# Optimization experiments

Measured on AMD Instinct MI355X. Metric: run time of the kernel, lower is better.

Reference implementation:

```python
import jax, jax.numpy as jnp
import numpy as np

B, S = 4096, 8192

def setup_inputs() -> dict:
    key = jax.random.key(0)
    c = jax.random.normal(key, (B, S), dtype=jnp.float32)
    beta = jnp.asarray(10.0, dtype=jnp.float32)
    return {"c": c, "beta": beta}

def reference(c, beta):
    # Original per-step recurrence:
    #   delta_i = (1/beta) * logsumexp([beta*delta_{i-1}, beta*(c_i + delta_{i-1})])
    #           = delta_{i-1} + (1/beta) * log(1 + exp(beta * c_i))
    # i.e. an exact prefix sum of softplus(beta*c)/beta along S.
    # (Note: the torch code stacks delta_prev, not 0, as the first branch,
    #  so the logsumexp telescopes to a cumulative sum.)
    step = jax.nn.softplus(beta * c) / beta          # (B, S)
    return jnp.cumsum(step, axis=1)                  # (B, S) propagated delays
```

## Files before the change

### kernel.cpp

```cpp
#include <hip/hip_runtime.h>


#define ROW_S   8192
#define NJ      4
#define PASS_F4 (64 * NJ)
#define NPASS   (ROW_S / (PASS_F4 * 4))
#define WPB     4
#define BLOCK_T (WPB * 64)

typedef float f32x4 __attribute__((ext_vector_type(4)));

__device__ __forceinline__ float softplus_step(float c, float beta, float inv_beta) {
    float tb = beta * c;
    float a  = fabsf(tb);
    float e  = __expf(-a);
    float l  = __logf(1.0f + e);
    return (fmaxf(tb, 0.0f) + l) * inv_beta;
}

__global__ __launch_bounds__(BLOCK_T, 4) void softplus_cumsum_kernel(
    const float* __restrict__ c,
    const float* __restrict__ beta_p,
    float* __restrict__ out,
    int nrows)
{
    const int lane = threadIdx.x & 63;
    const int wave = threadIdx.x >> 6;
    const int row  = blockIdx.x * WPB + wave;
    if (row >= nrows) return;

    const float beta     = beta_p[0];
    const float inv_beta = 1.0f / beta;

    const f32x4* __restrict__ in4  = (const f32x4*)c   + (size_t)row * (ROW_S / 4);
    f32x4*       __restrict__ out4 = (f32x4*)out       + (size_t)row * (ROW_S / 4);

    float carry = 0.0f;

    f32x4 va[NJ], vb[NJ];
    #pragma unroll
    for (int j = 0; j < NJ; ++j) va[j] = in4[0 * PASS_F4 + j * 64 + lane];
    #pragma unroll
    for (int j = 0; j < NJ; ++j) vb[j] = in4[1 * PASS_F4 + j * 64 + lane];

    auto body = [&](f32x4 (&cur)[NJ], const int p) {
        f32x4 r[NJ];
        float s[NJ];
        #pragma unroll
        for (int j = 0; j < NJ; ++j) {
            float a = softplus_step(cur[j].x, beta, inv_beta);
            float b = softplus_step(cur[j].y, beta, inv_beta);
            float d = softplus_step(cur[j].z, beta, inv_beta);
            float e = softplus_step(cur[j].w, beta, inv_beta);
            r[j].x = a;
            r[j].y = a + b;
            r[j].z = r[j].y + d;
            r[j].w = r[j].z + e;
            s[j]   = r[j].w;
        }

        if (p + 2 < NPASS) {
            #pragma unroll
            for (int j = 0; j < NJ; ++j)
                cur[j] = in4[(p + 2) * PASS_F4 + j * 64 + lane];
        }

        float xs[NJ], G[NJ];
        #pragma unroll
        for (int j = 0; j < NJ; ++j) {
            float x = s[j];
            #pragma unroll
            for (int d = 1; d < 64; d <<= 1) {
                float y = __shfl_up(x, d, 64);
                if (lane >= d) x += y;
            }
            xs[j] = x;
            G[j]  = __shfl(x, 63, 64);
        }

        float pre = carry;
        #pragma unroll
        for (int j = 0; j < NJ; ++j) {
            const float off = pre + (xs[j] - s[j]);
            pre += G[j];
            f32x4 o;
            o.x = r[j].x + off;
            o.y = r[j].y + off;
            o.z = r[j].z + off;
            o.w = r[j].w + off;
            out4[p * PASS_F4 + j * 64 + lane] = o;
        }
        carry = pre;
    };

    body(va, 0); body(vb, 1);
    body(va, 2); body(vb, 3);
    body(va, 4); body(vb, 5);
    body(va, 6); body(vb, 7);
}

extern "C" void kernel_launch(void* const* d_in, const int* in_sizes, int n_in,
                              void* d_out, int out_size, void* d_ws, size_t ws_size,
                              hipStream_t stream) {
    const float* c      = (const float*)d_in[0];
    const float* beta_p = (const float*)d_in[1];
    float*       out    = (float*)d_out;

    const int B    = in_sizes[0] / ROW_S;
    const int grid = (B + WPB - 1) / WPB;

    softplus_cumsum_kernel<<<dim3(grid), dim3(BLOCK_T), 0, stream>>>(
        c, beta_p, out, B);
}
```

Measured before the change: 240.6 us.

## Give each lane a contiguous 32-element chunk and do one wave scan per segment

Each lane now owns 8 contiguous float4 vectors inside a 2048-element segment and does a serial local scan over them. The row is covered in 4 segments instead of 8 passes, so the wave needs only one 64-lane shuffle scan per segment, down from four per pass. The catch is that each lane's loads and stores become strided by 128 bytes across lanes instead of fully coalesced, and the serial accumulation chain per lane is longer.

```diff
diff --git a/kernel.cpp b/kernel.cpp
--- a/kernel.cpp
+++ b/kernel.cpp
@@ -1,12 +1,13 @@
 #include <hip/hip_runtime.h>
 
 
-#define ROW_S   8192
-#define NJ      4
-#define PASS_F4 (64 * NJ)
-#define NPASS   (ROW_S / (PASS_F4 * 4))
-#define WPB     4
-#define BLOCK_T (WPB * 64)
+#define ROW_S    8192
+#define NSEG     4
+#define SEG_ELEM (ROW_S / NSEG)
+#define LANE_F4  8
+#define SEG_F4   (SEG_ELEM / 4)
+#define WPB      4
+#define BLOCK_T  (WPB * 64)
 
 typedef float f32x4 __attribute__((ext_vector_type(4)));
 
@@ -34,69 +35,57 @@
 
     const f32x4* __restrict__ in4  = (const f32x4*)c   + (size_t)row * (ROW_S / 4);
     f32x4*       __restrict__ out4 = (f32x4*)out       + (size_t)row * (ROW_S / 4);
+    const int lb = lane * LANE_F4;
 
     float carry = 0.0f;
 
-    f32x4 va[NJ], vb[NJ];
+    f32x4 va[LANE_F4], vb[LANE_F4];
     #pragma unroll
-    for (int j = 0; j < NJ; ++j) va[j] = in4[0 * PASS_F4 + j * 64 + lane];
+    for (int k = 0; k < LANE_F4; ++k) va[k] = in4[0 * SEG_F4 + lb + k];
     #pragma unroll
-    for (int j = 0; j < NJ; ++j) vb[j] = in4[1 * PASS_F4 + j * 64 + lane];
+    for (int k = 0; k < LANE_F4; ++k) vb[k] = in4[1 * SEG_F4 + lb + k];
 
-    auto body = [&](f32x4 (&cur)[NJ], const int p) {
-        f32x4 r[NJ];
-        float s[NJ];
+    auto body = [&](f32x4 (&cur)[LANE_F4], const int s) {
+        f32x4 r[LANE_F4];
+        float acc = 0.0f;
         #pragma unroll
-        for (int j = 0; j < NJ; ++j) {
-            float a = softplus_step(cur[j].x, beta, inv_beta);
-            float b = softplus_step(cur[j].y, beta, inv_beta);
-            float d = softplus_step(cur[j].z, beta, inv_beta);
-            float e = softplus_step(cur[j].w, beta, inv_beta);
-            r[j].x = a;
-            r[j].y = a + b;
-            r[j].z = r[j].y + d;
-            r[j].w = r[j].z + e;
-            s[j]   = r[j].w;
+        for (int k = 0; k < LANE_F4; ++k) {
+            acc += softplus_step(cur[k].x, beta, inv_beta);  r[k].x = acc;
+            acc += softplus_step(cur[k].y, beta, inv_beta);  r[k].y = acc;
+            acc += softplus_step(cur[k].z, beta, inv_beta);  r[k].z = acc;
+            acc += softplus_step(cur[k].w, beta, inv_beta);  r[k].w = acc;
+        }
+        const float total = acc;
+
+        if (s + 2 < NSEG) {
+            #pragma unroll
+            for (int k = 0; k < LANE_F4; ++k)
+                cur[k] = in4[(s + 2) * SEG_F4 + lb + k];
         }
 
-        if (p + 2 < NPASS) {
-            #pragma unroll
-            for (int j = 0; j < NJ; ++j)
-                cur[j] = in4[(p + 2) * PASS_F4 + j * 64 + lane];
+        float x = total;
+        #pragma unroll
+        for (int d = 1; d < 64; d <<= 1) {
+            float y = __shfl_up(x, d, 64);
+            if (lane >= d) x += y;
         }
+        const float off    = carry + (x - total);
+        const float segtot = __shfl(x, 63, 64);
+        carry += segtot;
 
-        float xs[NJ], G[NJ];
         #pragma unroll
-        for (int j = 0; j < NJ; ++j) {
-            float x = s[j];
-            #pragma unroll
-            for (int d = 1; d < 64; d <<= 1) {
-                float y = __shfl_up(x, d, 64);
-                if (lane >= d) x += y;
-            }
-            xs[j] = x;
-            G[j]  = __shfl(x, 63, 64);
+        for (int k = 0; k < LANE_F4; ++k) {
+            f32x4 o;
+            o.x = r[k].x + off;
+            o.y = r[k].y + off;
+            o.z = r[k].z + off;
+            o.w = r[k].w + off;
+            out4[s * SEG_F4 + lb + k] = o;
         }
-
-        float pre = carry;
-        #pragma unroll
-        for (int j = 0; j < NJ; ++j) {
-            const float off = pre + (xs[j] - s[j]);
-            pre += G[j];
-            f32x4 o;
-            o.x = r[j].x + off;
-            o.y = r[j].y + off;
-            o.z = r[j].z + off;
-            o.w = r[j].w + off;
-            out4[p * PASS_F4 + j * 64 + lane] = o;
-        }
-        carry = pre;
     };
 
     body(va, 0); body(vb, 1);
     body(va, 2); body(vb, 3);
-    body(va, 4); body(vb, 5);
-    body(va, 6); body(vb, 7);
 }
 
 extern "C" void kernel_launch(void* const* d_in, const int* in_sizes, int n_in,
```

Result: slower. 291.6 us (+21.2%).

## Split row scan into chunk-sum and scan-apply kernels over 1024-element chunks

Applied to the files above, without the earlier changes.

Replaces the one-wave-per-row sequential scan with a two-kernel reduce-then-scan. The first kernel computes per-chunk softplus sums and writes them to workspace. The second reads those sums, takes a per-chunk prefix, re-reads the input, and does an in-chunk scan. This exposes eight times more independent waves, but it reads the input twice and computes the softplus twice, which adds about 50% more memory traffic to a bandwidth-bound kernel.

```diff
diff --git a/kernel.cpp b/kernel.cpp
--- a/kernel.cpp
+++ b/kernel.cpp
@@ -2,9 +2,8 @@
 
 
 #define ROW_S   8192
-#define NJ      4
-#define PASS_F4 (64 * NJ)
-#define NPASS   (ROW_S / (PASS_F4 * 4))
+#define CHUNK   1024
+#define NCH     (ROW_S / CHUNK)
 #define WPB     4
 #define BLOCK_T (WPB * 64)
 
@@ -18,85 +17,115 @@
     return (fmaxf(tb, 0.0f) + l) * inv_beta;
 }
 
-__global__ __launch_bounds__(BLOCK_T, 4) void softplus_cumsum_kernel(
+__global__ __launch_bounds__(BLOCK_T) void chunk_sum_kernel(
     const float* __restrict__ c,
     const float* __restrict__ beta_p,
-    float* __restrict__ out,
-    int nrows)
+    float* __restrict__ sums,
+    int nchunks)
 {
     const int lane = threadIdx.x & 63;
     const int wave = threadIdx.x >> 6;
-    const int row  = blockIdx.x * WPB + wave;
-    if (row >= nrows) return;
+    const int gid  = blockIdx.x * WPB + wave;
+    if (gid >= nchunks) return;
+
+    const float beta     = beta_p[0];
+    const float inv_beta = 1.0f / beta;
+    const f32x4* __restrict__ in4 = (const f32x4*)c + (size_t)gid * (CHUNK / 4);
+
+    f32x4 v[4];
+    #pragma unroll
+    for (int j = 0; j < 4; ++j)
+        v[j] = in4[j * 64 + lane];
+
+    float s = 0.0f;
+    #pragma unroll
+    for (int j = 0; j < 4; ++j) {
+        s += softplus_step(v[j].x, beta, inv_beta);
+        s += softplus_step(v[j].y, beta, inv_beta);
+        s += softplus_step(v[j].z, beta, inv_beta);
+        s += softplus_step(v[j].w, beta, inv_beta);
+    }
+
+    #pragma unroll
+    for (int d = 1; d < 64; d <<= 1)
+        s += __shfl_xor(s, d, 64);
+
+    if (lane == 0) sums[gid] = s;
+}
+
+__global__ __launch_bounds__(BLOCK_T) void scan_apply_kernel(
+    const float* __restrict__ c,
+    const float* __restrict__ beta_p,
+    const float* __restrict__ sums,
+    float* __restrict__ out,
+    int nchunks)
+{
+    const int lane = threadIdx.x & 63;
+    const int wave = threadIdx.x >> 6;
+    const int gid  = blockIdx.x * WPB + wave;
+    if (gid >= nchunks) return;
+
+    const int jch     = gid & (NCH - 1);
+    const int rowbase = gid & ~(NCH - 1);
 
     const float beta     = beta_p[0];
     const float inv_beta = 1.0f / beta;
 
-    const f32x4* __restrict__ in4  = (const f32x4*)c   + (size_t)row * (ROW_S / 4);
-    f32x4*       __restrict__ out4 = (f32x4*)out       + (size_t)row * (ROW_S / 4);
+    float pre0 = 0.0f;
+    #pragma unroll
+    for (int k = 0; k < NCH; ++k) {
+        float w = sums[rowbase + k];
+        if (k < jch) pre0 += w;
+    }
 
-    float carry = 0.0f;
+    const f32x4* __restrict__ in4  = (const f32x4*)c   + (size_t)gid * (CHUNK / 4);
+    f32x4*       __restrict__ out4 = (f32x4*)out       + (size_t)gid * (CHUNK / 4);
 
-    f32x4 va[NJ], vb[NJ];
+    f32x4 v[4];
     #pragma unroll
-    for (int j = 0; j < NJ; ++j) va[j] = in4[0 * PASS_F4 + j * 64 + lane];
+    for (int j = 0; j < 4; ++j)
+        v[j] = in4[j * 64 + lane];
+
+    f32x4 r[4];
+    float s[4];
     #pragma unroll
-    for (int j = 0; j < NJ; ++j) vb[j] = in4[1 * PASS_F4 + j * 64 + lane];
+    for (int j = 0; j < 4; ++j) {
+        float a = softplus_step(v[j].x, beta, inv_beta);
+        float b = softplus_step(v[j].y, beta, inv_beta);
+        float d = softplus_step(v[j].z, beta, inv_beta);
+        float e = softplus_step(v[j].w, beta, inv_beta);
+        r[j].x = a;
+        r[j].y = a + b;
+        r[j].z = r[j].y + d;
+        r[j].w = r[j].z + e;
+        s[j]   = r[j].w;
+    }
 
-    auto body = [&](f32x4 (&cur)[NJ], const int p) {
-        f32x4 r[NJ];
-        float s[NJ];
+    float xs[4], G[4];
+    #pragma unroll
+    for (int j = 0; j < 4; ++j) {
+        float x = s[j];
         #pragma unroll
-        for (int j = 0; j < NJ; ++j) {
-            float a = softplus_step(cur[j].x, beta, inv_beta);
-            float b = softplus_step(cur[j].y, beta, inv_beta);
-            float d = softplus_step(cur[j].z, beta, inv_beta);
-            float e = softplus_step(cur[j].w, beta, inv_beta);
-            r[j].x = a;
-            r[j].y = a + b;
-            r[j].z = r[j].y + d;
-            r[j].w = r[j].z + e;
-            s[j]   = r[j].w;
+        for (int d = 1; d < 64; d <<= 1) {
+            float y = __shfl_up(x, d, 64);
+            if (lane >= d) x += y;
         }
+        xs[j] = x;
+        G[j]  = __shfl(x, 63, 64);
+    }
 
-        if (p + 2 < NPASS) {
-            #pragma unroll
-            for (int j = 0; j < NJ; ++j)
-                cur[j] = in4[(p + 2) * PASS_F4 + j * 64 + lane];
-        }
-
-        float xs[NJ], G[NJ];
-        #pragma unroll
-        for (int j = 0; j < NJ; ++j) {
-            float x = s[j];
-            #pragma unroll
-            for (int d = 1; d < 64; d <<= 1) {
-                float y = __shfl_up(x, d, 64);
-                if (lane >= d) x += y;
-            }
-            xs[j] = x;
-            G[j]  = __shfl(x, 63, 64);
-        }
-
-        float pre = carry;
-        #pragma unroll
-        for (int j = 0; j < NJ; ++j) {
-            const float off = pre + (xs[j] - s[j]);
-            pre += G[j];
-            f32x4 o;
-            o.x = r[j].x + off;
-            o.y = r[j].y + off;
-            o.z = r[j].z + off;
-            o.w = r[j].w + off;
-            out4[p * PASS_F4 + j * 64 + lane] = o;
-        }
-        carry = pre;
-    };
-
-    body(va, 0); body(vb, 1);
-    body(va, 2); body(vb, 3);
-    body(va, 4); body(vb, 5);
-    body(va, 6); body(vb, 7);
+    float pre = pre0;
+    #pragma unroll
+    for (int j = 0; j < 4; ++j) {
+        const float off = pre + (xs[j] - s[j]);
+        pre += G[j];
+        f32x4 o;
+        o.x = r[j].x + off;
+        o.y = r[j].y + off;
+        o.z = r[j].z + off;
+        o.w = r[j].w + off;
+        out4[j * 64 + lane] = o;
+    }
 }
 
 extern "C" void kernel_launch(void* const* d_in, const int* in_sizes, int n_in,
@@ -106,9 +135,14 @@
     const float* beta_p = (const float*)d_in[1];
     float*       out    = (float*)d_out;
 
-    const int B    = in_sizes[0] / ROW_S;
-    const int grid = (B + WPB - 1) / WPB;
+    const int B       = in_sizes[0] / ROW_S;
+    const int nchunks = B * NCH;
+    const int grid    = (nchunks + WPB - 1) / WPB;
 
-    softplus_cumsum_kernel<<<dim3(grid), dim3(BLOCK_T), 0, stream>>>(
-        c, beta_p, out, B);
+    float* sums = (float*)d_ws;
+
+    chunk_sum_kernel<<<dim3(grid), dim3(BLOCK_T), 0, stream>>>(
+        c, beta_p, sums, nchunks);
+    scan_apply_kernel<<<dim3(grid), dim3(BLOCK_T), 0, stream>>>(
+        c, beta_p, sums, out, nchunks);
 }
```

Measured after the change: 246.5 us. 1.02x slower.
